# Performance work log

Hardware: AMD Instinct MI355X
Metric: run time of the kernel (lower is better)

## Reference

```python
import jax, jax.numpy as jnp
import numpy as np

N = 50000      # nodes
E = 800000     # edges (before self-loops)
IN = 128       # in_channels
HID = 32       # hidden_channels
H = 4          # heads (hidden layers)
H_LAST = 6     # heads of final conv (concat=False -> mean)
OUT = 2        # out_channels
NEG = 0.2      # LeakyReLU slope in GATConv


def setup_inputs() -> dict:
    key = jax.random.key(0)
    ks = jax.random.split(key, 24)
    r = lambda k, s, sc=0.1: (jax.random.normal(k, s, jnp.float32) * sc)
    inp = {
        "x": jax.random.normal(ks[0], (N, IN), jnp.float32),
        "edge_index": jax.random.randint(ks[1], (2, E), 0, N, dtype=jnp.int32),
        "edge_attr": jax.random.normal(ks[2], (E, 1), jnp.float32),  # ignored by GATConv (edge_dim=None)
        # layer 0: GATConv(IN -> HID, heads=H, concat) + Linear(IN -> HID*H)
        "c0_W": r(ks[3], (IN, H * HID)), "c0_as": r(ks[4], (H, HID)), "c0_ad": r(ks[5], (H, HID)), "c0_b": jnp.zeros((H * HID,), jnp.float32),
        "l0_W": r(ks[6], (IN, H * HID)), "l0_b": jnp.zeros((H * HID,), jnp.float32),
        # layer 1 (middle): GATConv(HID*H -> HID, heads=H) + Linear(HID*H -> HID*H)
        "c1_W": r(ks[7], (H * HID, H * HID)), "c1_as": r(ks[8], (H, HID)), "c1_ad": r(ks[9], (H, HID)), "c1_b": jnp.zeros((H * HID,), jnp.float32),
        "l1_W": r(ks[10], (H * HID, H * HID)), "l1_b": jnp.zeros((H * HID,), jnp.float32),
        # layer 2 (last): GATConv(HID*H -> OUT, heads=H_LAST, concat=False) + Linear(HID*H -> OUT)
        "c2_W": r(ks[11], (H * HID, H_LAST * OUT)), "c2_as": r(ks[12], (H_LAST, OUT)), "c2_ad": r(ks[13], (H_LAST, OUT)), "c2_b": jnp.zeros((OUT,), jnp.float32),
        "l2_W": r(ks[14], (H * HID, OUT)), "l2_b": jnp.zeros((OUT,), jnp.float32),
    }
    return inp


def gat_conv(x, src, dst, W, a_src, a_dst, b, heads, ch, concat):
    n = x.shape[0]
    xw = (x @ W).reshape(n, heads, ch)                      # [N,H,C]
    al_s = jnp.einsum('nhc,hc->nh', xw, a_src)              # [N,H]
    al_d = jnp.einsum('nhc,hc->nh', xw, a_dst)
    alpha = jax.nn.leaky_relu(al_s[src] + al_d[dst], NEG)   # [E,H]
    # segment softmax over edges sharing the same destination node
    m = jax.ops.segment_max(alpha, dst, num_segments=n)
    e = jnp.exp(alpha - m[dst])
    s = jax.ops.segment_sum(e, dst, num_segments=n)
    coef = e / s[dst]                                       # [E,H]
    out = jax.ops.segment_sum(xw[src] * coef[:, :, None], dst, num_segments=n)  # [N,H,C]
    out = out.reshape(n, heads * ch) if concat else out.mean(axis=1)
    return out + b


def reference(x, edge_index, edge_attr,
              c0_W, c0_as, c0_ad, c0_b, l0_W, l0_b,
              c1_W, c1_as, c1_ad, c1_b, l1_W, l1_b,
              c2_W, c2_as, c2_ad, c2_b, l2_W, l2_b):
    n = x.shape[0]
    loops = jnp.arange(n, dtype=edge_index.dtype)  # GATConv add_self_loops=True
    src = jnp.concatenate([edge_index[0], loops])
    dst = jnp.concatenate([edge_index[1], loops])
    # edge_attr is ignored: GATConv built without edge_dim has lin_edge=None
    h = jax.nn.relu(gat_conv(x, src, dst, c0_W, c0_as, c0_ad, c0_b, H, HID, True) + x @ l0_W + l0_b)
    h = jax.nn.relu(gat_conv(h, src, dst, c1_W, c1_as, c1_ad, c1_b, H, HID, True) + h @ l1_W + l1_b)
    out = gat_conv(h, src, dst, c2_W, c2_as, c2_ad, c2_b, H_LAST, OUT, False) + h @ l2_W + l2_b
    return out
```

## Files before the change

### kernel.cpp

```cpp
#include <hip/hip_runtime.h>
#include <hip/hip_bf16.h>


#define NEG_SLOPE 0.2f
#define SC_CHUNK 4096
#define CAP 64

typedef __attribute__((ext_vector_type(8))) short short8;
typedef __attribute__((ext_vector_type(4))) float floatx4;

static __device__ __forceinline__ float leaky(float x) {
    return x > 0.f ? x : NEG_SLOPE * x;
}

static __device__ __forceinline__ unsigned short f2bf(float f) {
    unsigned int u = __float_as_uint(f);
    u = (u + 0x7fffu + ((u >> 16) & 1u)) >> 16;
    return (unsigned short)u;
}

static __device__ __forceinline__ unsigned int pack_bf2(float lo, float hi) {
    return (unsigned int)f2bf(lo) | ((unsigned int)f2bf(hi) << 16);
}

static __device__ __forceinline__ float bflo(unsigned int u) {
    return __uint_as_float(u << 16);
}
static __device__ __forceinline__ float bfhi(unsigned int u) {
    return __uint_as_float(u & 0xffff0000u);
}

__global__ __launch_bounds__(256) void k_bucket(
    const int* __restrict__ ei, int E, int N, int rs,
    int* __restrict__ cnt, int* __restrict__ col) {
    int lo = blockIdx.x * rs, hi = lo + rs;
    int base = blockIdx.y * SC_CHUNK;
    int ET = E + N;
#pragma unroll 4
    for (int o = threadIdx.x; o < SC_CHUNK; o += 256) {
        int e = base + o;
        if (e >= ET) break;
        int d = (e < E) ? ei[E + e] : (e - E);
        if (d < lo || d >= hi) continue;
        int s = (e < E) ? ei[e] : d;
        int pos = atomicAdd(&cnt[d], 1);
        if (pos < CAP) col[(d << 6) + pos] = s;
    }
}


__global__ void k_conv_x(const float* __restrict__ x, unsigned short* __restrict__ Ab,
                         int N, int Mpad) {
    int t = blockIdx.x * 256 + threadIdx.x;
    if (t >= Mpad * 32) return;
    int r = t >> 5;
    float4 v = make_float4(0.f, 0.f, 0.f, 0.f);
    if (r < N) v = ((const float4*)x)[t];
    ushort4 o;
    o.x = f2bf(v.x); o.y = f2bf(v.y); o.z = f2bf(v.z); o.w = f2bf(v.w);
    ((ushort4*)Ab)[t] = o;
}

__global__ void k_conv_w(const float* W0, unsigned short* T0,
                         const float* W1, unsigned short* T1,
                         const float* W2, unsigned short* T2,
                         const float* W3, unsigned short* T3,
                         const float* c2W, const float* l2W, unsigned short* WT5) {
    int t = blockIdx.x * 256 + threadIdx.x;
    if (blockIdx.y == 4) {
        if (t >= 2048) return;
        int n = t >> 7, k = t & 127;
        float v = 0.f;
        if (n < 12) v = c2W[k * 12 + n];
        else if (n < 14) v = l2W[k * 2 + (n - 12)];
        WT5[n * 128 + k] = f2bf(v);
        return;
    }
    const float* W; unsigned short* T;
    switch (blockIdx.y) {
        case 0: W = W0; T = T0; break;
        case 1: W = W1; T = T1; break;
        case 2: W = W2; T = T2; break;
        default: W = W3; T = T3; break;
    }
    int n = t >> 7, k = t & 127;
    T[n * 128 + k] = f2bf(W[k * 128 + n]);
}

__global__ __launch_bounds__(256) void k_gemm_mfma(
    const unsigned short* __restrict__ Ab,
    const unsigned short* __restrict__ W1T,
    unsigned int* __restrict__ XWb,
    const float* __restrict__ a_s, const float* __restrict__ a_d,
    float4* __restrict__ ALS4, float4* __restrict__ ALD4,
    const unsigned short* __restrict__ W2T,
    const float* __restrict__ b2,
    unsigned short* __restrict__ Hsb,
    int M) {
    int which = blockIdx.y;
    const unsigned short* WT = which ? W2T : W1T;
    int row0 = blockIdx.x * 64;
    int w = threadIdx.x >> 6, lane = threadIdx.x & 63;
    int m = lane & 15, q = lane >> 4;

    const short8* A8 = (const short8*)Ab;
    const short8* W8 = (const short8*)WT;

    floatx4 acc[8];
#pragma unroll
    for (int ct = 0; ct < 8; ct++) acc[ct] = (floatx4){0.f, 0.f, 0.f, 0.f};

    int arow = row0 + w * 16 + m;
#pragma unroll
    for (int ks = 0; ks < 4; ks++) {
        short8 afrag = A8[arow * 16 + ks * 4 + q];
#pragma unroll
        for (int ct = 0; ct < 8; ct++) {
            short8 bfrag = W8[(ct * 16 + m) * 16 + ks * 4 + q];
            acc[ct] = __builtin_amdgcn_mfma_f32_16x16x32_bf16(afrag, bfrag, acc[ct], 0, 0, 0);
        }
    }

    int crow0 = row0 + w * 16 + q * 4;
    if (which) {
#pragma unroll
        for (int ct = 0; ct < 8; ct++) {
            int gc = ct * 16 + m;
            float bias = b2[gc];
#pragma unroll
            for (int r = 0; r < 4; r++) {
                int gr = crow0 + r;
                if (gr < M) Hsb[gr * 128 + gc] = f2bf(acc[ct][r] + bias);
            }
        }
    } else {
#pragma unroll
        for (int ct = 0; ct < 4; ct++) {
#pragma unroll
            for (int r = 0; r < 4; r++) {
                int gr = crow0 + r;
                if (gr < M)
                    XWb[gr * 64 + ct * 16 + m] = pack_bf2(acc[ct][r], acc[ct + 4][r]);
            }
        }
        float sv[4][4], dv[4][4];
#pragma unroll
        for (int h = 0; h < 4; h++) {
            float as0 = a_s[h * 32 + m], as1 = a_s[h * 32 + 16 + m];
            float ad0 = a_d[h * 32 + m], ad1 = a_d[h * 32 + 16 + m];
#pragma unroll
            for (int r = 0; r < 4; r++) {
                sv[h][r] = acc[2 * h][r] * as0 + acc[2 * h + 1][r] * as1;
                dv[h][r] = acc[2 * h][r] * ad0 + acc[2 * h + 1][r] * ad1;
            }
        }
#pragma unroll
        for (int off = 8; off >= 1; off >>= 1) {
#pragma unroll
            for (int h = 0; h < 4; h++)
#pragma unroll
                for (int r = 0; r < 4; r++) {
                    sv[h][r] += __shfl_xor(sv[h][r], off);
                    dv[h][r] += __shfl_xor(dv[h][r], off);
                }
        }
        if (m == 0) {
#pragma unroll
            for (int r = 0; r < 4; r++) {
                int gr = crow0 + r;
                if (gr < M) {
                    ALS4[gr] = make_float4(sv[0][r], sv[1][r], sv[2][r], sv[3][r]);
                    ALD4[gr] = make_float4(dv[0][r], dv[1][r], dv[2][r], dv[3][r]);
                }
            }
        }
    }
}

__global__ __launch_bounds__(256) void k_gemm_small(
    const unsigned short* __restrict__ Ab,
    const unsigned short* __restrict__ WT5,
    float* __restrict__ C14) {
    int w = threadIdx.x >> 6, lane = threadIdx.x & 63;
    int m = lane & 15, q = lane >> 4;
    const short8* A8 = (const short8*)Ab;
    const short8* W8 = (const short8*)WT5;
    floatx4 acc = (floatx4){0.f, 0.f, 0.f, 0.f};
    int arow = blockIdx.x * 64 + w * 16 + m;
#pragma unroll
    for (int ks = 0; ks < 4; ks++) {
        short8 afrag = A8[arow * 16 + ks * 4 + q];
        short8 bfrag = W8[m * 16 + ks * 4 + q];
        acc = __builtin_amdgcn_mfma_f32_16x16x32_bf16(afrag, bfrag, acc, 0, 0, 0);
    }
    int crow0 = blockIdx.x * 64 + w * 16 + q * 4;
#pragma unroll
    for (int r = 0; r < 4; r++)
        C14[(crow0 + r) * 16 + m] = acc[r];
}

__global__ __launch_bounds__(256) void k_agg4(
    const int* __restrict__ cntv, const int* __restrict__ col,
    const uint4* __restrict__ XWb4,
    const float4* __restrict__ ALS4, const float4* __restrict__ ALD4,
    const float* __restrict__ cb,
    const unsigned short* __restrict__ Hsb, unsigned short* __restrict__ Hb, int N) {
    int wid = threadIdx.x >> 6, lane = threadIdx.x & 63;
    int node = blockIdx.x * 4 + wid;
    if (node >= N) return;
    int deg = cntv[node];
    if (deg > CAP) deg = CAP;
    int start = node << 6;
    int gq = lane >> 4, g = lane & 15;
    int hA = g >> 3;
    float4 ad = ALD4[node];
    float adA = hA ? ad.y : ad.x;
    float adB = hA ? ad.w : ad.z;

    float a0 = 0.f, a1 = 0.f, a2 = 0.f, a3 = 0.f;
    float b0 = 0.f, b1 = 0.f, b2 = 0.f, b3 = 0.f;
    float sA = 0.f, sB = 0.f;
    int i = 0;
    for (; i + 8 <= deg; i += 8) {
        int s0 = col[start + i + gq];
        int s1 = col[start + i + 4 + gq];
        float4 as0 = ALS4[s0], as1 = ALS4[s1];
        uint4 u0 = XWb4[(size_t)s0 * 16 + g];
        uint4 u1 = XWb4[(size_t)s1 * 16 + g];
        float eA0 = __expf(leaky((hA ? as0.y : as0.x) + adA));
        float eB0 = __expf(leaky((hA ? as0.w : as0.z) + adB));
        float eA1 = __expf(leaky((hA ? as1.y : as1.x) + adA));
        float eB1 = __expf(leaky((hA ? as1.w : as1.z) + adB));
        sA += eA0 + eA1; sB += eB0 + eB1;
        a0 += eA0 * bflo(u0.x) + eA1 * bflo(u1.x);
        b0 += eB0 * bfhi(u0.x) + eB1 * bfhi(u1.x);
        a1 += eA0 * bflo(u0.y) + eA1 * bflo(u1.y);
        b1 += eB0 * bfhi(u0.y) + eB1 * bfhi(u1.y);
        a2 += eA0 * bflo(u0.z) + eA1 * bflo(u1.z);
        b2 += eB0 * bfhi(u0.z) + eB1 * bfhi(u1.z);
        a3 += eA0 * bflo(u0.w) + eA1 * bflo(u1.w);
        b3 += eB0 * bfhi(u0.w) + eB1 * bfhi(u1.w);
    }
    for (; i + 4 <= deg; i += 4) {
        int s0 = col[start + i + gq];
        float4 as0 = ALS4[s0];
        uint4 u0 = XWb4[(size_t)s0 * 16 + g];
        float eA0 = __expf(leaky((hA ? as0.y : as0.x) + adA));
        float eB0 = __expf(leaky((hA ? as0.w : as0.z) + adB));
        sA += eA0; sB += eB0;
        a0 += eA0 * bflo(u0.x); b0 += eB0 * bfhi(u0.x);
        a1 += eA0 * bflo(u0.y); b1 += eB0 * bfhi(u0.y);
        a2 += eA0 * bflo(u0.z); b2 += eB0 * bfhi(u0.z);
        a3 += eA0 * bflo(u0.w); b3 += eB0 * bfhi(u0.w);
    }
    int rem = deg - i;
    if (gq < rem) {
        int s0 = col[start + i + gq];
        float4 as0 = ALS4[s0];
        uint4 u0 = XWb4[(size_t)s0 * 16 + g];
        float eA0 = __expf(leaky((hA ? as0.y : as0.x) + adA));
        float eB0 = __expf(leaky((hA ? as0.w : as0.z) + adB));
        sA += eA0; sB += eB0;
        a0 += eA0 * bflo(u0.x); b0 += eB0 * bfhi(u0.x);
        a1 += eA0 * bflo(u0.y); b1 += eB0 * bfhi(u0.y);
        a2 += eA0 * bflo(u0.z); b2 += eB0 * bfhi(u0.z);
        a3 += eA0 * bflo(u0.w); b3 += eB0 * bfhi(u0.w);
    }
#define RED2(v) { v += __shfl_xor(v, 16); v += __shfl_xor(v, 32); }
    RED2(sA) RED2(sB)
    RED2(a0) RED2(a1) RED2(a2) RED2(a3)
    RED2(b0) RED2(b1) RED2(b2) RED2(b3)
#undef RED2

    if (gq == 0) {
        float invA = 1.f / sA, invB = 1.f / sB;
        float4 cl = ((const float4*)cb)[g];
        float4 ch = ((const float4*)cb)[g + 16];
        uint2 skl = ((const uint2*)(Hsb + node * 128))[g];
        uint2 skh = ((const uint2*)(Hsb + node * 128 + 64))[g];
        float v0 = a0 * invA + cl.x + bflo(skl.x);
        float v1 = a1 * invA + cl.y + bfhi(skl.x);
        float v2 = a2 * invA + cl.z + bflo(skl.y);
        float v3 = a3 * invA + cl.w + bfhi(skl.y);
        float w0 = b0 * invB + ch.x + bflo(skh.x);
        float w1 = b1 * invB + ch.y + bfhi(skh.x);
        float w2 = b2 * invB + ch.z + bflo(skh.y);
        float w3 = b3 * invB + ch.w + bfhi(skh.y);
        v0 = v0 > 0.f ? v0 : 0.f;  v1 = v1 > 0.f ? v1 : 0.f;
        v2 = v2 > 0.f ? v2 : 0.f;  v3 = v3 > 0.f ? v3 : 0.f;
        w0 = w0 > 0.f ? w0 : 0.f;  w1 = w1 > 0.f ? w1 : 0.f;
        w2 = w2 > 0.f ? w2 : 0.f;  w3 = w3 > 0.f ? w3 : 0.f;
        uint2 ol, oh;
        ol.x = pack_bf2(v0, v1); ol.y = pack_bf2(v2, v3);
        oh.x = pack_bf2(w0, w1); oh.y = pack_bf2(w2, w3);
        ((uint2*)(Hb + node * 128))[g] = ol;
        ((uint2*)(Hb + node * 128 + 64))[g] = oh;
    }
}

__global__ void k_l2post(const float* __restrict__ C14,
                         const float* __restrict__ c2as, const float* __restrict__ c2ad,
                         const float* __restrict__ l2b,
                         float* __restrict__ L2D, float* __restrict__ ALD2,
                         float* __restrict__ out, int N) {
    int n = blockIdx.x * 256 + threadIdx.x;
    if (n >= N) return;
    const float4* c4 = (const float4*)(C14 + n * 16);
    float4 p0 = c4[0], p1 = c4[1], p2 = c4[2], p3 = c4[3];
    float p[12] = {p0.x, p0.y, p0.z, p0.w, p1.x, p1.y, p1.z, p1.w,
                   p2.x, p2.y, p2.z, p2.w};
    float als[6], ald[6];
#pragma unroll
    for (int h = 0; h < 6; h++) {
        als[h] = p[2 * h] * c2as[2 * h] + p[2 * h + 1] * c2as[2 * h + 1];
        ald[h] = p[2 * h] * c2ad[2 * h] + p[2 * h + 1] * c2ad[2 * h + 1];
    }
    float4* rec = (float4*)(L2D + n * 20);
    rec[0] = p0; rec[1] = p1; rec[2] = p2;
    rec[3] = make_float4(als[0], als[1], als[2], als[3]);
    rec[4] = make_float4(als[4], als[5], 0.f, 0.f);
    float4* ad4 = (float4*)(ALD2 + n * 8);
    ad4[0] = make_float4(ald[0], ald[1], ald[2], ald[3]);
    ad4[1] = make_float4(ald[4], ald[5], 0.f, 0.f);
    out[n * 2 + 0] = p3.x + l2b[0];
    out[n * 2 + 1] = p3.y + l2b[1];
}

__global__ __launch_bounds__(256) void k_agg2(
    const int* __restrict__ cntv, const int* __restrict__ col,
    const float4* __restrict__ L2D4,
    const float* __restrict__ ALD2,
    const float* __restrict__ c2b,
    float* __restrict__ out, int N) {
    int g = threadIdx.x >> 4, l = threadIdx.x & 15;
    int node = blockIdx.x * 16 + g;
    if (node >= N) return;
    int deg = cntv[node];
    if (deg > CAP) deg = CAP;
    int start = node << 6;

    float ald[6];
    {
        float4 d03 = *(const float4*)(ALD2 + node * 8);
        float2 d45 = *(const float2*)(ALD2 + node * 8 + 4);
        ald[0] = d03.x; ald[1] = d03.y; ald[2] = d03.z; ald[3] = d03.w;
        ald[4] = d45.x; ald[5] = d45.y;
    }

    float se[6], a0[6], a1[6];
#pragma unroll
    for (int h = 0; h < 6; h++) { se[h] = 0.f; a0[h] = 0.f; a1[h] = 0.f; }

    for (int i = l; i < deg; i += 16) {
        int s = col[start + i];
        float4 x03 = L2D4[s * 5 + 0];
        float4 x47 = L2D4[s * 5 + 1];
        float4 x8b = L2D4[s * 5 + 2];
        float4 as03 = L2D4[s * 5 + 3];
        float4 as45 = L2D4[s * 5 + 4];
        float als[6] = {as03.x, as03.y, as03.z, as03.w, as45.x, as45.y};
        float xw[12] = {x03.x, x03.y, x03.z, x03.w, x47.x, x47.y, x47.z, x47.w,
                        x8b.x, x8b.y, x8b.z, x8b.w};
#pragma unroll
        for (int h = 0; h < 6; h++) {
            float e = __expf(leaky(als[h] + ald[h]));
            se[h] += e;
            a0[h] += e * xw[2 * h];
            a1[h] += e * xw[2 * h + 1];
        }
    }
#pragma unroll
    for (int m = 8; m >= 1; m >>= 1) {
#pragma unroll
        for (int h = 0; h < 6; h++) {
            se[h] += __shfl_xor(se[h], m);
            a0[h] += __shfl_xor(a0[h], m);
            a1[h] += __shfl_xor(a1[h], m);
        }
    }
    if (l == 0) {
        float o0 = 0.f, o1 = 0.f;
#pragma unroll
        for (int h = 0; h < 6; h++) {
            float inv = 1.f / se[h];
            o0 += a0[h] * inv;
            o1 += a1[h] * inv;
        }
        out[node * 2 + 0] += o0 * (1.f / 6.f) + c2b[0];
        out[node * 2 + 1] += o1 * (1.f / 6.f) + c2b[1];
    }
}


extern "C" void kernel_launch(void* const* d_in, const int* in_sizes, int n_in,
                              void* d_out, int out_size, void* d_ws, size_t ws_size,
                              hipStream_t stream) {
    const float* x   = (const float*)d_in[0];
    const int* ei    = (const int*)d_in[1];
    const float* c0W = (const float*)d_in[3];
    const float* c0as = (const float*)d_in[4];
    const float* c0ad = (const float*)d_in[5];
    const float* c0b = (const float*)d_in[6];
    const float* l0W = (const float*)d_in[7];
    const float* l0b = (const float*)d_in[8];
    const float* c1W = (const float*)d_in[9];
    const float* c1as = (const float*)d_in[10];
    const float* c1ad = (const float*)d_in[11];
    const float* c1b = (const float*)d_in[12];
    const float* l1W = (const float*)d_in[13];
    const float* l1b = (const float*)d_in[14];
    const float* c2W = (const float*)d_in[15];
    const float* c2as = (const float*)d_in[16];
    const float* c2ad = (const float*)d_in[17];
    const float* c2b = (const float*)d_in[18];
    const float* l2W = (const float*)d_in[19];
    const float* l2b = (const float*)d_in[20];
    float* out = (float*)d_out;

    const int N = in_sizes[0] / 128;
    const int E = in_sizes[1] / 2;
    const int ET = E + N;
    const int Mpad = (N + 63) & ~63;

    char* p = (char*)d_ws;
    auto alloc = [&](size_t bytes) -> void* {
        void* r = (void*)p;
        p += (bytes + 255) & ~(size_t)255;
        return r;
    };
    unsigned short* Hsb = (unsigned short*)alloc((size_t)N * 128 * 2);
    unsigned int* XWb = (unsigned int*)alloc((size_t)N * 64 * 4);
    unsigned short* Ab = (unsigned short*)alloc((size_t)Mpad * 128 * 2);
    unsigned short* W1T = (unsigned short*)alloc(128 * 128 * 2);
    unsigned short* W2T = (unsigned short*)alloc(128 * 128 * 2);
    unsigned short* W3T = (unsigned short*)alloc(128 * 128 * 2);
    unsigned short* W4T = (unsigned short*)alloc(128 * 128 * 2);
    unsigned short* WT5 = (unsigned short*)alloc(16 * 128 * 2);
    float* ALS = (float*)alloc((size_t)N * 4 * 4);
    float* ALD = (float*)alloc((size_t)N * 8 * 4);
    float* L2D = (float*)alloc((size_t)N * 20 * 4);
    float* C14 = (float*)alloc((size_t)Mpad * 16 * 4);
    int* cnt    = (int*)alloc((size_t)N * 4);
    int* col    = (int*)alloc((size_t)N * CAP * 4);

    const int nb = (N + 255) / 256;

    hipMemsetAsync(cnt, 0, (size_t)N * 4, stream);
    int rs = (N + 7) / 8;
    dim3 bgrid(8, (ET + SC_CHUNK - 1) / SC_CHUNK);
    k_bucket<<<bgrid, 256, 0, stream>>>(ei, E, N, rs, cnt, col);

    k_conv_x<<<(Mpad * 32 + 255) / 256, 256, 0, stream>>>(x, Ab, N, Mpad);
    dim3 wgrid(64, 5);
    k_conv_w<<<wgrid, 256, 0, stream>>>(c0W, W1T, l0W, W2T, c1W, W3T, l1W, W4T,
                                        c2W, l2W, WT5);

    dim3 ggrid(Mpad / 64, 2);
    int nwb = (N + 3) / 4;

    k_gemm_mfma<<<ggrid, 256, 0, stream>>>(Ab, W1T, XWb, c0as, c0ad,
                                           (float4*)ALS, (float4*)ALD,
                                           W2T, l0b, Hsb, N);
    k_agg4<<<nwb, 256, 0, stream>>>(cnt, col, (const uint4*)XWb,
                                    (const float4*)ALS, (const float4*)ALD,
                                    c0b, Hsb, Ab, N);

    k_gemm_mfma<<<ggrid, 256, 0, stream>>>(Ab, W3T, XWb, c1as, c1ad,
                                           (float4*)ALS, (float4*)ALD,
                                           W4T, l1b, Hsb, N);
    k_agg4<<<nwb, 256, 0, stream>>>(cnt, col, (const uint4*)XWb,
                                    (const float4*)ALS, (const float4*)ALD,
                                    c1b, Hsb, Ab, N);

    k_gemm_small<<<Mpad / 64, 256, 0, stream>>>(Ab, WT5, C14);
    k_l2post<<<nb, 256, 0, stream>>>(C14, c2as, c2ad, l2b, L2D, ALD, out, N);
    k_agg2<<<(N + 15) / 16, 256, 0, stream>>>(cnt, col, (const float4*)L2D,
                                              ALD, c2b, out, N);
}
```

Measured before the change: 334.0 us.

## Fuse final-layer postprocess into small GEMM and prefetch neighbor lists

Folds the k_l2post attention-logit and output-bias computation into the epilogue of k_gemm_small, using a lane shuffle to sum head pairs. This drops the C14 intermediate buffer and one kernel launch. k_agg4 now loads all 64 column indices per wave at once and broadcasts them with shuffles, with the inner loop unrolled to four edges per step. k_agg2 preloads its four index slots before doing any gathers. The padding slots of L2D and ALD2 are no longer written, which is harmless only because they are never read.

Result: no change. 332.1 us (-0.6%).

```diff
diff --git a/kernel.cpp b/kernel.cpp
--- a/kernel.cpp
+++ b/kernel.cpp
@@ -180,7 +180,10 @@
 __global__ __launch_bounds__(256) void k_gemm_small(
     const unsigned short* __restrict__ Ab,
     const unsigned short* __restrict__ WT5,
-    float* __restrict__ C14) {
+    const float* __restrict__ c2as, const float* __restrict__ c2ad,
+    const float* __restrict__ l2b,
+    float* __restrict__ L2D, float* __restrict__ ALD2,
+    float* __restrict__ out, int M) {
     int w = threadIdx.x >> 6, lane = threadIdx.x & 63;
     int m = lane & 15, q = lane >> 4;
     const short8* A8 = (const short8*)Ab;
@@ -193,10 +196,37 @@
         short8 bfrag = W8[m * 16 + ks * 4 + q];
         acc = __builtin_amdgcn_mfma_f32_16x16x32_bf16(afrag, bfrag, acc, 0, 0, 0);
     }
+    float asm_ = (m < 12) ? c2as[m] : 0.f;
+    float adm  = (m < 12) ? c2ad[m] : 0.f;
     int crow0 = blockIdx.x * 64 + w * 16 + q * 4;
-#pragma unroll
-    for (int r = 0; r < 4; r++)
-        C14[(crow0 + r) * 16 + m] = acc[r];
+    float sc[4], dc[4];
+#pragma unroll
+    for (int r = 0; r < 4; r++) {
+        sc[r] = acc[r] * asm_;
+        dc[r] = acc[r] * adm;
+    }
+#pragma unroll
+    for (int r = 0; r < 4; r++) {
+        sc[r] += __shfl_xor(sc[r], 1);
+        dc[r] += __shfl_xor(dc[r], 1);
+    }
+#pragma unroll
+    for (int r = 0; r < 4; r++) {
+        int gr = crow0 + r;
+        if (gr >= M) continue;
+        if (m < 12) {
+            L2D[gr * 20 + m] = acc[r];
+            if ((m & 1) == 0) {
+                int h = m >> 1;
+                L2D[gr * 20 + 12 + h] = sc[r];
+                ALD2[gr * 8 + h] = dc[r];
+            }
+        } else if (m == 12) {
+            out[gr * 2 + 0] = acc[r] + l2b[0];
+        } else if (m == 13) {
+            out[gr * 2 + 1] = acc[r] + l2b[1];
+        }
+    }
 }
 
 __global__ __launch_bounds__(256) void k_agg4(
@@ -213,6 +243,7 @@
     int start = node << 6;
     int gq = lane >> 4, g = lane & 15;
     int hA = g >> 3;
+    int cval = col[start + lane];
     float4 ad = ALD4[node];
     float adA = hA ? ad.y : ad.x;
     float adB = hA ? ad.w : ad.z;
@@ -220,52 +251,39 @@
     float a0 = 0.f, a1 = 0.f, a2 = 0.f, a3 = 0.f;
     float b0 = 0.f, b1 = 0.f, b2 = 0.f, b3 = 0.f;
     float sA = 0.f, sB = 0.f;
+
+#define EDGE(sv)                                                       \
+    {                                                                  \
+        float4 as = ALS4[sv];                                          \
+        uint4 u = XWb4[(size_t)(sv) * 16 + g];                         \
+        float eA = __expf(leaky((hA ? as.y : as.x) + adA));            \
+        float eB = __expf(leaky((hA ? as.w : as.z) + adB));            \
+        sA += eA; sB += eB;                                            \
+        a0 += eA * bflo(u.x); b0 += eB * bfhi(u.x);                    \
+        a1 += eA * bflo(u.y); b1 += eB * bfhi(u.y);                    \
+        a2 += eA * bflo(u.z); b2 += eB * bfhi(u.z);                    \
+        a3 += eA * bflo(u.w); b3 += eB * bfhi(u.w);                    \
+    }
+
     int i = 0;
-    for (; i + 8 <= deg; i += 8) {
-        int s0 = col[start + i + gq];
-        int s1 = col[start + i + 4 + gq];
-        float4 as0 = ALS4[s0], as1 = ALS4[s1];
-        uint4 u0 = XWb4[(size_t)s0 * 16 + g];
-        uint4 u1 = XWb4[(size_t)s1 * 16 + g];
-        float eA0 = __expf(leaky((hA ? as0.y : as0.x) + adA));
-        float eB0 = __expf(leaky((hA ? as0.w : as0.z) + adB));
-        float eA1 = __expf(leaky((hA ? as1.y : as1.x) + adA));
-        float eB1 = __expf(leaky((hA ? as1.w : as1.z) + adB));
-        sA += eA0 + eA1; sB += eB0 + eB1;
-        a0 += eA0 * bflo(u0.x) + eA1 * bflo(u1.x);
-        b0 += eB0 * bfhi(u0.x) + eB1 * bfhi(u1.x);
-        a1 += eA0 * bflo(u0.y) + eA1 * bflo(u1.y);
-        b1 += eB0 * bfhi(u0.y) + eB1 * bfhi(u1.y);
-        a2 += eA0 * bflo(u0.z) + eA1 * bflo(u1.z);
-        b2 += eB0 * bfhi(u0.z) + eB1 * bfhi(u1.z);
-        a3 += eA0 * bflo(u0.w) + eA1 * bflo(u1.w);
-        b3 += eB0 * bfhi(u0.w) + eB1 * bfhi(u1.w);
+    for (; i + 16 <= deg; i += 16) {
+        int s0 = __shfl(cval, i + gq);
+        int s1 = __shfl(cval, i + 4 + gq);
+        int s2 = __shfl(cval, i + 8 + gq);
+        int s3 = __shfl(cval, i + 12 + gq);
+        EDGE(s0) EDGE(s1) EDGE(s2) EDGE(s3)
     }
     for (; i + 4 <= deg; i += 4) {
-        int s0 = col[start + i + gq];
-        float4 as0 = ALS4[s0];
-        uint4 u0 = XWb4[(size_t)s0 * 16 + g];
-        float eA0 = __expf(leaky((hA ? as0.y : as0.x) + adA));
-        float eB0 = __expf(leaky((hA ? as0.w : as0.z) + adB));
-        sA += eA0; sB += eB0;
-        a0 += eA0 * bflo(u0.x); b0 += eB0 * bfhi(u0.x);
-        a1 += eA0 * bflo(u0.y); b1 += eB0 * bfhi(u0.y);
-        a2 += eA0 * bflo(u0.z); b2 += eB0 * bfhi(u0.z);
-        a3 += eA0 * bflo(u0.w); b3 += eB0 * bfhi(u0.w);
+        int s0 = __shfl(cval, i + gq);
+        EDGE(s0)
     }
     int rem = deg - i;
-    if (gq < rem) {
-        int s0 = col[start + i + gq];
-        float4 as0 = ALS4[s0];
-        uint4 u0 = XWb4[(size_t)s0 * 16 + g];
-        float eA0 = __expf(leaky((hA ? as0.y : as0.x) + adA));
-        float eB0 = __expf(leaky((hA ? as0.w : as0.z) + adB));
-        sA += eA0; sB += eB0;
-        a0 += eA0 * bflo(u0.x); b0 += eB0 * bfhi(u0.x);
-        a1 += eA0 * bflo(u0.y); b1 += eB0 * bfhi(u0.y);
-        a2 += eA0 * bflo(u0.z); b2 += eB0 * bfhi(u0.z);
-        a3 += eA0 * bflo(u0.w); b3 += eB0 * bfhi(u0.w);
-    }
+    if (rem > 0) {
+        int s0 = __shfl(cval, i + (gq < rem ? gq : 0));
+        if (gq < rem) EDGE(s0)
+    }
+#undef EDGE
+
 #define RED2(v) { v += __shfl_xor(v, 16); v += __shfl_xor(v, 32); }
     RED2(sA) RED2(sB)
     RED2(a0) RED2(a1) RED2(a2) RED2(a3)
@@ -298,34 +316,6 @@
     }
 }
 
-__global__ void k_l2post(const float* __restrict__ C14,
-                         const float* __restrict__ c2as, const float* __restrict__ c2ad,
-                         const float* __restrict__ l2b,
-                         float* __restrict__ L2D, float* __restrict__ ALD2,
-                         float* __restrict__ out, int N) {
-    int n = blockIdx.x * 256 + threadIdx.x;
-    if (n >= N) return;
-    const float4* c4 = (const float4*)(C14 + n * 16);
-    float4 p0 = c4[0], p1 = c4[1], p2 = c4[2], p3 = c4[3];
-    float p[12] = {p0.x, p0.y, p0.z, p0.w, p1.x, p1.y, p1.z, p1.w,
-                   p2.x, p2.y, p2.z, p2.w};
-    float als[6], ald[6];
-#pragma unroll
-    for (int h = 0; h < 6; h++) {
-        als[h] = p[2 * h] * c2as[2 * h] + p[2 * h + 1] * c2as[2 * h + 1];
-        ald[h] = p[2 * h] * c2ad[2 * h] + p[2 * h + 1] * c2ad[2 * h + 1];
-    }
-    float4* rec = (float4*)(L2D + n * 20);
-    rec[0] = p0; rec[1] = p1; rec[2] = p2;
-    rec[3] = make_float4(als[0], als[1], als[2], als[3]);
-    rec[4] = make_float4(als[4], als[5], 0.f, 0.f);
-    float4* ad4 = (float4*)(ALD2 + n * 8);
-    ad4[0] = make_float4(ald[0], ald[1], ald[2], ald[3]);
-    ad4[1] = make_float4(ald[4], ald[5], 0.f, 0.f);
-    out[n * 2 + 0] = p3.x + l2b[0];
-    out[n * 2 + 1] = p3.y + l2b[1];
-}
-
 __global__ __launch_bounds__(256) void k_agg2(
     const int* __restrict__ cntv, const int* __restrict__ col,
     const float4* __restrict__ L2D4,
@@ -339,6 +329,11 @@
     if (deg > CAP) deg = CAP;
     int start = node << 6;
 
+    int c0 = (l      < deg) ? col[start + l]      : -1;
+    int c1 = (l + 16 < deg) ? col[start + l + 16] : -1;
+    int c2 = (l + 32 < deg) ? col[start + l + 32] : -1;
+    int c3 = (l + 48 < deg) ? col[start + l + 48] : -1;
+
     float ald[6];
     {
         float4 d03 = *(const float4*)(ALD2 + node * 8);
@@ -351,24 +346,28 @@
 #pragma unroll
     for (int h = 0; h < 6; h++) { se[h] = 0.f; a0[h] = 0.f; a1[h] = 0.f; }
 
-    for (int i = l; i < deg; i += 16) {
-        int s = col[start + i];
-        float4 x03 = L2D4[s * 5 + 0];
-        float4 x47 = L2D4[s * 5 + 1];
-        float4 x8b = L2D4[s * 5 + 2];
-        float4 as03 = L2D4[s * 5 + 3];
-        float4 as45 = L2D4[s * 5 + 4];
-        float als[6] = {as03.x, as03.y, as03.z, as03.w, as45.x, as45.y};
-        float xw[12] = {x03.x, x03.y, x03.z, x03.w, x47.x, x47.y, x47.z, x47.w,
-                        x8b.x, x8b.y, x8b.z, x8b.w};
-#pragma unroll
-        for (int h = 0; h < 6; h++) {
-            float e = __expf(leaky(als[h] + ald[h]));
-            se[h] += e;
-            a0[h] += e * xw[2 * h];
-            a1[h] += e * xw[2 * h + 1];
-        }
-    }
+#define EDGE2(sv)                                                          \
+    if ((sv) >= 0) {                                                       \
+        float4 x03 = L2D4[(sv) * 5 + 0];                                   \
+        float4 x47 = L2D4[(sv) * 5 + 1];                                   \
+        float4 x8b = L2D4[(sv) * 5 + 2];                                   \
+        float4 as03 = L2D4[(sv) * 5 + 3];                                  \
+        float4 as45 = L2D4[(sv) * 5 + 4];                                  \
+        float als[6] = {as03.x, as03.y, as03.z, as03.w, as45.x, as45.y};   \
+        float xw[12] = {x03.x, x03.y, x03.z, x03.w, x47.x, x47.y, x47.z,   \
+                        x47.w, x8b.x, x8b.y, x8b.z, x8b.w};                \
+        _Pragma("unroll")                                                  \
+        for (int h = 0; h < 6; h++) {                                      \
+            float e = __expf(leaky(als[h] + ald[h]));                      \
+            se[h] += e;                                                    \
+            a0[h] += e * xw[2 * h];                                        \
+            a1[h] += e * xw[2 * h + 1];                                    \
+        }                                                                  \
+    }
+
+    EDGE2(c0) EDGE2(c1) EDGE2(c2) EDGE2(c3)
+#undef EDGE2
+
 #pragma unroll
     for (int m = 8; m >= 1; m >>= 1) {
 #pragma unroll
@@ -439,11 +438,8 @@
     float* ALS = (float*)alloc((size_t)N * 4 * 4);
     float* ALD = (float*)alloc((size_t)N * 8 * 4);
     float* L2D = (float*)alloc((size_t)N * 20 * 4);
-    float* C14 = (float*)alloc((size_t)Mpad * 16 * 4);
     int* cnt    = (int*)alloc((size_t)N * 4);
     int* col    = (int*)alloc((size_t)N * CAP * 4);
-
-    const int nb = (N + 255) / 256;
 
     hipMemsetAsync(cnt, 0, (size_t)N * 4, stream);
     int rs = (N + 7) / 8;
@@ -472,8 +468,8 @@
                                     (const float4*)ALS, (const float4*)ALD,
                                     c1b, Hsb, Ab, N);
 
-    k_gemm_small<<<Mpad / 64, 256, 0, stream>>>(Ab, WT5, C14);
-    k_l2post<<<nb, 256, 0, stream>>>(C14, c2as, c2ad, l2b, L2D, ALD, out, N);
+    k_gemm_small<<<Mpad / 64, 256, 0, stream>>>(Ab, WT5, c2as, c2ad, l2b,
+                                                L2D, ALD, out, N);
     k_agg2<<<(N + 15) / 16, 256, 0, stream>>>(cnt, col, (const float4*)L2D,
                                               ALD, c2b, out, N);
 }
```
